# Kernel optimization log

Hardware: AMD Instinct MI355X
Metric: run time of the kernel (lower is better)

The kernel has to match this reference:

```python
import jax, jax.numpy as jnp
import numpy as np

H = 0.5
EPS = 1e-08


def setup_inputs() -> dict:
    key = jax.random.key(0)
    k1, k2, k3 = jax.random.split(key, 3)
    B, in_dim, n_rules, out_dim = 16384, 64, 128, 32
    X = jax.random.normal(k1, (B, in_dim), dtype=jnp.float32)
    centers = jax.random.normal(k2, (in_dim, n_rules), dtype=jnp.float32)
    sigmas = jnp.ones((in_dim, n_rules), dtype=jnp.float32)
    W = jax.random.normal(k3, (out_dim, (in_dim + 1) * n_rules), dtype=jnp.float32) * 0.02
    b = jnp.zeros((out_dim,), dtype=jnp.float32)
    return {"X": X, "centers": centers, "sigmas": sigmas, "W": W, "b": b}


def reference(X, centers, sigmas, W, b):
    # HTSK firing levels: mean-style scaled Gaussian log-memberships summed over in_dim
    scale = H / sigmas ** 2 + EPS                      # [in_dim, n_rules]
    diff = X[:, :, None] - centers[None, :, :]          # [B, in_dim, n_rules]
    logits = jnp.sum(-(diff ** 2) * scale, axis=1)      # [B, n_rules]
    frs = jax.nn.softmax(logits, axis=1)                # [B, n_rules]
    B = X.shape[0]
    # order=1 consequent input: rule-major outer product, then raw firing levels
    xr = (frs[:, :, None] * X[:, None, :]).reshape(B, -1)  # [B, n_rules*in_dim]
    Z = jnp.concatenate([xr, frs], axis=1)               # [B, n_rules*(in_dim+1)]
    output = Z @ W.T + b                                 # [B, out_dim]
    return output, frs
```

## Files before the change

kernel.cpp:

```cpp
#include <hip/hip_runtime.h>


#define H_CONST 0.5f
#define EPS_CONST 1e-8f
#define NROWS 16384
#define NRULES 128
#define WCOLS 8320

typedef _Float16 half8 __attribute__((ext_vector_type(8)));
typedef float floatx4 __attribute__((ext_vector_type(4)));

#define MFMA16(a, b, c) __builtin_amdgcn_mfma_f32_16x16x32_f16((a), (b), (c), 0, 0, 0)

#define WFRAG_OFF 0
#define W0FRAG_OFF 262144
#define BMAT_OFF   (262144 + 4096)
#define KVEC_BYTE_OFF 630784
#define WS_BYTES_NEEDED (630784 + 512)

__global__ __launch_bounds__(256) void prep_kernel(
    const float* __restrict__ centers, const float* __restrict__ sigmas,
    const float* __restrict__ W, _Float16* __restrict__ wsh, float* __restrict__ kvec)
{
    __shared__ float sBuf[32 * 68];
    const int t = threadIdx.x;
    const int b = blockIdx.x;

    if (b < 128) {
        const int r = b;
        {
            int o = t >> 3, seg = t & 7;
            const float* g = W + o * WCOLS + r * 64 + seg * 8;
            floatx4 a = *(const floatx4*)g;
            floatx4 c = *(const floatx4*)(g + 4);
            *(floatx4*)(sBuf + o * 68 + seg * 8) = a;
            *(floatx4*)(sBuf + o * 68 + seg * 8 + 4) = c;
        }
        __syncthreads();
        {
            int L = t & 63, nt = (t >> 6) & 1, s = t >> 7;
            int o = nt * 16 + (L & 15);
            int ib = s * 32 + ((L >> 4) & 3) * 8;
            floatx4 fa = *(const floatx4*)(sBuf + o * 68 + ib);
            floatx4 fb = *(const floatx4*)(sBuf + o * 68 + ib + 4);
            half8 h;
#pragma unroll
            for (int k = 0; k < 8; ++k) h[k] = (_Float16)((k < 4) ? fa[k & 3] : fb[k & 3]);
            *(half8*)(wsh + WFRAG_OFF + r * 2048 + t * 8) = h;
        }
    } else if (b < 136) {
        const int nt = b - 128;
        float* sS = sBuf;
        float* sC = sBuf + 1088;
        {
            int i = t >> 2, c0 = (t & 3) * 4;
            floatx4 sg4 = *(const floatx4*)(sigmas + i * NRULES + nt * 16 + c0);
            floatx4 ct4 = *(const floatx4*)(centers + i * NRULES + nt * 16 + c0);
#pragma unroll
            for (int k = 0; k < 4; ++k) { sS[i * 17 + c0 + k] = sg4[k]; sC[i * 17 + c0 + k] = ct4[k]; }
        }
        __syncthreads();
#pragma unroll
        for (int kk = 0; kk < 3; ++kk) {
            int unit = t + kk * 256;
            int s = unit >> 6, L = unit & 63;
            int q = (L >> 4) & 3, nl = L & 15;
            int g = s >> 1;
            int i0 = (s & 1) * 32 + q * 8;
            half8 h;
#pragma unroll
            for (int j = 0; j < 8; ++j) {
                int i = i0 + j;
                float sg = sS[i * 17 + nl];
                float S = H_CONST / (sg * sg) + EPS_CONST;
                float c = sC[i * 17 + nl];
                float CS2 = 2.0f * c * S;
                _Float16 v;
                if (g == 0 || g == 2) v = -(_Float16)S;
                else if (g == 1) { _Float16 sh = (_Float16)S; v = -(_Float16)(S - (float)sh); }
                else if (g == 3 || g == 5) v = (_Float16)CS2;
                else { _Float16 ch = (_Float16)CS2; v = (_Float16)(CS2 - (float)ch); }
                h[j] = v;
            }
            *(half8*)(wsh + BMAT_OFF + ((s * 8 + nt) * 64 + L) * 8) = h;
        }
    } else {
#pragma unroll
        for (int kk = 0; kk < 2; ++kk) {
            int unit = t + kk * 256;
            int s = unit >> 7, nt = (unit >> 6) & 1, L = unit & 63;
            int q = (L >> 4) & 3;
            int o = nt * 16 + (L & 15);
            half8 h;
#pragma unroll
            for (int j = 0; j < 8; ++j) {
                int r = s * 32 + q * 8 + j;
                h[j] = (_Float16)W[o * WCOLS + 8192 + r];
            }
            *(half8*)(wsh + W0FRAG_OFF + ((s * 2 + nt) * 64 + L) * 8) = h;
        }
        if (t < 128) {
            int r = t;
            float acc = 0.f;
#pragma unroll 8
            for (int i = 0; i < 64; ++i) {
                float sg = sigmas[i * NRULES + r];
                float S = H_CONST / (sg * sg) + EPS_CONST;
                float c = centers[i * NRULES + r];
                acc += c * c * S;
            }
            kvec[r] = acc;
        }
    }
}

__global__ __launch_bounds__(256) void main_fused(
    const float* __restrict__ X, const float* __restrict__ bias,
    const _Float16* __restrict__ wsh, const float* __restrict__ kvec,
    float* __restrict__ out, float* __restrict__ frs_out)
{
    __shared__ _Float16 sXh[32 * 64];
    __shared__ _Float16 sXl[32 * 64];
    __shared__ _Float16 sX2h[32 * 64];
    __shared__ _Float16 sX2l[32 * 64];
    __shared__ float sU[32 * 132];
    __shared__ _Float16 sF[32 * 136];

    const int t = threadIdx.x;
    const int w = t >> 6;
    const int L = t & 63;
    const int m = L & 15;
    const int q = L >> 4;
    const int row0 = blockIdx.x * 32;

    {
        int row = t >> 3, uc = t & 7;
        const float* gx = X + (row0 + row) * 64 + uc * 8;
        floatx4 xa = *(const floatx4*)gx;
        floatx4 xb = *(const floatx4*)(gx + 4);
        int base = row * 64 + (uc ^ (row & 7)) * 8;
        half8 vh, vl, v2h, v2l;
#pragma unroll
        for (int k = 0; k < 8; ++k) {
            float x = (k < 4) ? xa[k & 3] : xb[k & 3];
            _Float16 xh = (_Float16)x;
            _Float16 xl2 = (_Float16)(x - (float)xh);
            float x2 = x * x;
            _Float16 x2h = (_Float16)x2;
            _Float16 x2l = (_Float16)(x2 - (float)x2h);
            vh[k] = xh; vl[k] = xl2; v2h[k] = x2h; v2l[k] = x2l;
        }
        *(half8*)(sXh + base) = vh;
        *(half8*)(sXl + base) = vl;
        *(half8*)(sX2h + base) = v2h;
        *(half8*)(sX2l + base) = v2l;
    }
    __syncthreads();

    floatx4 lacc[2][2];
#pragma unroll
    for (int mt = 0; mt < 2; ++mt)
#pragma unroll
        for (int n = 0; n < 2; ++n) lacc[mt][n] = (floatx4){0.f, 0.f, 0.f, 0.f};

    const _Float16* Bm = wsh + BMAT_OFF;
#pragma unroll
    for (int s = 0; s < 12; ++s) {
        const _Float16* arr = (s < 4) ? sX2h : (s < 6) ? sX2l : (s < 10) ? sXh : sXl;
        int phys = (((s & 1) << 2) | q) ^ (m & 7);
        half8 b0 = *(const half8*)(Bm + ((s * 8 + 2 * w + 0) * 64 + L) * 8);
        half8 b1 = *(const half8*)(Bm + ((s * 8 + 2 * w + 1) * 64 + L) * 8);
#pragma unroll
        for (int mt = 0; mt < 2; ++mt) {
            half8 a = *(const half8*)(arr + (mt * 16 + m) * 64 + phys * 8);
            lacc[mt][0] = MFMA16(a, b0, lacc[mt][0]);
            lacc[mt][1] = MFMA16(a, b1, lacc[mt][1]);
        }
    }
    float kv0 = kvec[(2 * w + 0) * 16 + m];
    float kv1 = kvec[(2 * w + 1) * 16 + m];

#pragma unroll
    for (int mt = 0; mt < 2; ++mt)
#pragma unroll
        for (int ntl = 0; ntl < 2; ++ntl)
#pragma unroll
            for (int reg = 0; reg < 4; ++reg) {
                int rl = mt * 16 + q * 4 + reg;
                int col = (2 * w + ntl) * 16 + m;
                sU[rl * 132 + col] = lacc[mt][ntl][reg] - (ntl ? kv1 : kv0);
            }
    __syncthreads();

    {
        int row = t >> 3, l8 = t & 7;
        int base = row * 132 + l8 * 16;
        float v[16];
        float mx = -1e30f;
#pragma unroll
        for (int k = 0; k < 16; ++k) { v[k] = sU[base + k]; mx = fmaxf(mx, v[k]); }
        mx = fmaxf(mx, __shfl_xor(mx, 1));
        mx = fmaxf(mx, __shfl_xor(mx, 2));
        mx = fmaxf(mx, __shfl_xor(mx, 4));
        float sum = 0.f;
#pragma unroll
        for (int k = 0; k < 16; ++k) { v[k] = __expf(v[k] - mx); sum += v[k]; }
        sum += __shfl_xor(sum, 1);
        sum += __shfl_xor(sum, 2);
        sum += __shfl_xor(sum, 4);
        float inv = 1.0f / sum;
        float* gf = frs_out + (row0 + row) * 128 + l8 * 16;
        half8 h0, h1;
#pragma unroll
        for (int c = 0; c < 4; ++c) {
            floatx4 o4;
#pragma unroll
            for (int k = 0; k < 4; ++k) {
                float f = v[c * 4 + k] * inv;
                o4[k] = f;
                if (c < 2) h0[c * 4 + k] = (_Float16)f; else h1[(c - 2) * 4 + k] = (_Float16)f;
            }
            *(floatx4*)(gf + c * 4) = o4;
        }
        *(half8*)(sF + row * 136 + l8 * 16) = h0;
        *(half8*)(sF + row * 136 + l8 * 16 + 8) = h1;
    }
    __syncthreads();

    const int mt = w & 1;
    const int rh = w >> 1;

    half8 xf[2];
#pragma unroll
    for (int s = 0; s < 2; ++s) {
        int phys = ((s << 2) | q) ^ (m & 7);
        xf[s] = *(const half8*)(sXh + (mt * 16 + m) * 64 + phys * 8);
    }

    floatx4 oacc[2];
    oacc[0] = (floatx4){0.f, 0.f, 0.f, 0.f};
    oacc[1] = (floatx4){0.f, 0.f, 0.f, 0.f};

    const _Float16* Wf = wsh + WFRAG_OFF;
    const _Float16* W0f = wsh + W0FRAG_OFF;
    const int rowi = mt * 16 + m;

#pragma unroll 4
    for (int rr = 0; rr < 64; ++rr) {
        int r = rh * 64 + rr;
        const _Float16* bp = Wf + r * 2048;
        half8 b00 = *(const half8*)(bp + (0 * 64 + L) * 8);
        half8 b01 = *(const half8*)(bp + (1 * 64 + L) * 8);
        half8 b10 = *(const half8*)(bp + (2 * 64 + L) * 8);
        half8 b11 = *(const half8*)(bp + (3 * 64 + L) * 8);
        _Float16 f = sF[rowi * 136 + r];
        half8 fs;
#pragma unroll
        for (int k = 0; k < 8; ++k) fs[k] = f;
        half8 a0 = fs * xf[0];
        half8 a1 = fs * xf[1];
        oacc[0] = MFMA16(a0, b00, oacc[0]);
        oacc[0] = MFMA16(a1, b10, oacc[0]);
        oacc[1] = MFMA16(a0, b01, oacc[1]);
        oacc[1] = MFMA16(a1, b11, oacc[1]);
    }

#pragma unroll
    for (int sg = 0; sg < 2; ++sg) {
        int s = 2 * rh + sg;
        half8 a = *(const half8*)(sF + rowi * 136 + s * 32 + q * 8);
        half8 b0 = *(const half8*)(W0f + ((s * 2 + 0) * 64 + L) * 8);
        half8 b1 = *(const half8*)(W0f + ((s * 2 + 1) * 64 + L) * 8);
        oacc[0] = MFMA16(a, b0, oacc[0]);
        oacc[1] = MFMA16(a, b1, oacc[1]);
    }

    float* sR = sU;
    if (rh == 1) {
#pragma unroll
        for (int ntl = 0; ntl < 2; ++ntl)
#pragma unroll
            for (int reg = 0; reg < 4; ++reg)
                sR[(mt * 16 + q * 4 + reg) * 33 + ntl * 16 + m] = oacc[ntl][reg];
    }
    __syncthreads();
    if (rh == 0) {
        float b0 = bias[m];
        float b1 = bias[16 + m];
#pragma unroll
        for (int ntl = 0; ntl < 2; ++ntl) {
            float bb = ntl ? b1 : b0;
#pragma unroll
            for (int reg = 0; reg < 4; ++reg) {
                int rloc = mt * 16 + q * 4 + reg;
                int col = ntl * 16 + m;
                float vv = oacc[ntl][reg] + sR[rloc * 33 + col] + bb;
                out[(row0 + rloc) * 32 + col] = vv;
            }
        }
    }
}

extern "C" void kernel_launch(void* const* d_in, const int* in_sizes, int n_in,
                              void* d_out, int out_size, void* d_ws, size_t ws_size,
                              hipStream_t stream) {
    const float* X = (const float*)d_in[0];
    const float* centers = (const float*)d_in[1];
    const float* sigmas = (const float*)d_in[2];
    const float* W = (const float*)d_in[3];
    const float* b = (const float*)d_in[4];
    float* outp = (float*)d_out;
    float* frs_out = outp + NROWS * 32;
    if (ws_size < (size_t)WS_BYTES_NEEDED) return;
    _Float16* wsh = (_Float16*)d_ws;
    float* kvec = (float*)((char*)d_ws + KVEC_BYTE_OFF);

    prep_kernel<<<137, 256, 0, stream>>>(centers, sigmas, W, wsh, kvec);
    main_fused<<<NROWS / 32, 256, 0, stream>>>(X, b, wsh, kvec, outp, frs_out);
}
```

Measured before the change: 92.85 us.

## Split rules across four waves with both row tiles per wave and W prefetch

```diff
diff --git a/kernel.cpp b/kernel.cpp
--- a/kernel.cpp
+++ b/kernel.cpp
@@ -20,7 +20,7 @@
 
 __global__ __launch_bounds__(256) void prep_kernel(
     const float* __restrict__ centers, const float* __restrict__ sigmas,
-    const float* __restrict__ W, _Float16* __restrict__ wsh, float* __restrict__ kvec)
+    const float* __restrict__ W, _Float16* __restrict__ wsh)
 {
     __shared__ float sBuf[32 * 68];
     const int t = threadIdx.x;
@@ -99,19 +99,23 @@
             }
             *(half8*)(wsh + W0FRAG_OFF + ((s * 2 + nt) * 64 + L) * 8) = h;
         }
-        if (t < 128) {
-            int r = t;
-            float acc = 0.f;
+    }
+}
+
+__global__ __launch_bounds__(128) void prep_kvec(
+    const float* __restrict__ centers, const float* __restrict__ sigmas,
+    float* __restrict__ kvec)
+{
+    int r = threadIdx.x;
+    float acc = 0.f;
 #pragma unroll 8
-            for (int i = 0; i < 64; ++i) {
-                float sg = sigmas[i * NRULES + r];
-                float S = H_CONST / (sg * sg) + EPS_CONST;
-                float c = centers[i * NRULES + r];
-                acc += c * c * S;
-            }
-            kvec[r] = acc;
-        }
-    }
+    for (int i = 0; i < 64; ++i) {
+        float sg = sigmas[i * NRULES + r];
+        float S = H_CONST / (sg * sg) + EPS_CONST;
+        float c = centers[i * NRULES + r];
+        acc += c * c * S;
+    }
+    kvec[r] = acc;
 }
 
 __global__ __launch_bounds__(256) void main_fused(
@@ -123,8 +127,8 @@
     __shared__ _Float16 sXl[32 * 64];
     __shared__ _Float16 sX2h[32 * 64];
     __shared__ _Float16 sX2l[32 * 64];
-    __shared__ float sU[32 * 132];
     __shared__ _Float16 sF[32 * 136];
+    __shared__ float sU[4608];
 
     const int t = threadIdx.x;
     const int w = t >> 6;
@@ -227,78 +231,90 @@
     }
     __syncthreads();
 
-    const int mt = w & 1;
-    const int rh = w >> 1;
-
-    half8 xf[2];
-#pragma unroll
-    for (int s = 0; s < 2; ++s) {
-        int phys = ((s << 2) | q) ^ (m & 7);
-        xf[s] = *(const half8*)(sXh + (mt * 16 + m) * 64 + phys * 8);
-    }
-
-    floatx4 oacc[2];
-    oacc[0] = (floatx4){0.f, 0.f, 0.f, 0.f};
-    oacc[1] = (floatx4){0.f, 0.f, 0.f, 0.f};
-
+    const int rq = w;
+    const int r0 = rq * 32;
     const _Float16* Wf = wsh + WFRAG_OFF;
     const _Float16* W0f = wsh + W0FRAG_OFF;
-    const int rowi = mt * 16 + m;
-
-#pragma unroll 4
-    for (int rr = 0; rr < 64; ++rr) {
-        int r = rh * 64 + rr;
-        const _Float16* bp = Wf + r * 2048;
-        half8 b00 = *(const half8*)(bp + (0 * 64 + L) * 8);
-        half8 b01 = *(const half8*)(bp + (1 * 64 + L) * 8);
-        half8 b10 = *(const half8*)(bp + (2 * 64 + L) * 8);
-        half8 b11 = *(const half8*)(bp + (3 * 64 + L) * 8);
-        _Float16 f = sF[rowi * 136 + r];
-        half8 fs;
-#pragma unroll
-        for (int k = 0; k < 8; ++k) fs[k] = f;
-        half8 a0 = fs * xf[0];
-        half8 a1 = fs * xf[1];
-        oacc[0] = MFMA16(a0, b00, oacc[0]);
-        oacc[0] = MFMA16(a1, b10, oacc[0]);
-        oacc[1] = MFMA16(a0, b01, oacc[1]);
-        oacc[1] = MFMA16(a1, b11, oacc[1]);
-    }
-
-#pragma unroll
-    for (int sg = 0; sg < 2; ++sg) {
-        int s = 2 * rh + sg;
-        half8 a = *(const half8*)(sF + rowi * 136 + s * 32 + q * 8);
-        half8 b0 = *(const half8*)(W0f + ((s * 2 + 0) * 64 + L) * 8);
-        half8 b1 = *(const half8*)(W0f + ((s * 2 + 1) * 64 + L) * 8);
-        oacc[0] = MFMA16(a, b0, oacc[0]);
-        oacc[1] = MFMA16(a, b1, oacc[1]);
-    }
-
-    float* sR = sU;
-    if (rh == 1) {
+
+#define LDW(r, slot) (*(const half8*)(Wf + (r) * 2048 + ((slot) * 64 + L) * 8))
+
+    half8 xf[2][2];
+#pragma unroll
+    for (int mt = 0; mt < 2; ++mt)
+#pragma unroll
+        for (int s = 0; s < 2; ++s) {
+            int phys = ((s << 2) | q) ^ (m & 7);
+            xf[mt][s] = *(const half8*)(sXh + (mt * 16 + m) * 64 + phys * 8);
+        }
+
+    floatx4 oacc[2][2];
+#pragma unroll
+    for (int mt = 0; mt < 2; ++mt)
+#pragma unroll
+        for (int n = 0; n < 2; ++n) oacc[mt][n] = (floatx4){0.f, 0.f, 0.f, 0.f};
+
+    half8 b00 = LDW(r0, 0), b01 = LDW(r0, 1), b10 = LDW(r0, 2), b11 = LDW(r0, 3);
+
+#pragma unroll
+    for (int rg = 0; rg < 4; ++rg) {
+        half8 fv0 = *(const half8*)(sF + (0 * 16 + m) * 136 + r0 + rg * 8);
+        half8 fv1 = *(const half8*)(sF + (1 * 16 + m) * 136 + r0 + rg * 8);
+#pragma unroll
+        for (int rr2 = 0; rr2 < 8; ++rr2) {
+            half8 c00 = b00, c01 = b01, c10 = b10, c11 = b11;
+            if (rg * 8 + rr2 < 31) {
+                int rn = r0 + rg * 8 + rr2 + 1;
+                b00 = LDW(rn, 0); b01 = LDW(rn, 1); b10 = LDW(rn, 2); b11 = LDW(rn, 3);
+            }
+            _Float16 f0 = fv0[rr2], f1 = fv1[rr2];
+            half8 fs0, fs1;
+#pragma unroll
+            for (int k = 0; k < 8; ++k) { fs0[k] = f0; fs1[k] = f1; }
+            half8 a00 = fs0 * xf[0][0];
+            half8 a01 = fs0 * xf[0][1];
+            half8 a10 = fs1 * xf[1][0];
+            half8 a11 = fs1 * xf[1][1];
+            oacc[0][0] = MFMA16(a00, c00, oacc[0][0]);
+            oacc[0][0] = MFMA16(a01, c10, oacc[0][0]);
+            oacc[0][1] = MFMA16(a00, c01, oacc[0][1]);
+            oacc[0][1] = MFMA16(a01, c11, oacc[0][1]);
+            oacc[1][0] = MFMA16(a10, c00, oacc[1][0]);
+            oacc[1][0] = MFMA16(a11, c10, oacc[1][0]);
+            oacc[1][1] = MFMA16(a10, c01, oacc[1][1]);
+            oacc[1][1] = MFMA16(a11, c11, oacc[1][1]);
+        }
+    }
+
+    {
+        half8 wb0 = *(const half8*)(W0f + ((rq * 2 + 0) * 64 + L) * 8);
+        half8 wb1 = *(const half8*)(W0f + ((rq * 2 + 1) * 64 + L) * 8);
+#pragma unroll
+        for (int mt = 0; mt < 2; ++mt) {
+            half8 a = *(const half8*)(sF + (mt * 16 + m) * 136 + rq * 32 + q * 8);
+            oacc[mt][0] = MFMA16(a, wb0, oacc[mt][0]);
+            oacc[mt][1] = MFMA16(a, wb1, oacc[mt][1]);
+        }
+    }
+
+#pragma unroll
+    for (int mt = 0; mt < 2; ++mt)
 #pragma unroll
         for (int ntl = 0; ntl < 2; ++ntl)
 #pragma unroll
             for (int reg = 0; reg < 4; ++reg)
-                sR[(mt * 16 + q * 4 + reg) * 33 + ntl * 16 + m] = oacc[ntl][reg];
-    }
+                sU[w * 1152 + (mt * 16 + q * 4 + reg) * 36 + ntl * 16 + m] = oacc[mt][ntl][reg];
     __syncthreads();
-    if (rh == 0) {
-        float b0 = bias[m];
-        float b1 = bias[16 + m];
-#pragma unroll
-        for (int ntl = 0; ntl < 2; ++ntl) {
-            float bb = ntl ? b1 : b0;
-#pragma unroll
-            for (int reg = 0; reg < 4; ++reg) {
-                int rloc = mt * 16 + q * 4 + reg;
-                int col = ntl * 16 + m;
-                float vv = oacc[ntl][reg] + sR[rloc * 33 + col] + bb;
-                out[(row0 + rloc) * 32 + col] = vv;
-            }
-        }
-    }
+
+    {
+        int row = t >> 3, col0 = (t & 7) * 4;
+        floatx4 acc = *(const floatx4*)(sU + 0 * 1152 + row * 36 + col0);
+        acc += *(const floatx4*)(sU + 1 * 1152 + row * 36 + col0);
+        acc += *(const floatx4*)(sU + 2 * 1152 + row * 36 + col0);
+        acc += *(const floatx4*)(sU + 3 * 1152 + row * 36 + col0);
+        acc += *(const floatx4*)(bias + col0);
+        *(floatx4*)(out + (row0 + row) * 32 + col0) = acc;
+    }
+#undef LDW
 }
 
 extern "C" void kernel_launch(void* const* d_in, const int* in_sizes, int n_in,
@@ -315,6 +331,7 @@
     _Float16* wsh = (_Float16*)d_ws;
     float* kvec = (float*)((char*)d_ws + KVEC_BYTE_OFF);
 
-    prep_kernel<<<137, 256, 0, stream>>>(centers, sigmas, W, wsh, kvec);
+    prep_kernel<<<137, 256, 0, stream>>>(centers, sigmas, W, wsh);
+    prep_kvec<<<1, 128, 0, stream>>>(centers, sigmas, kvec);
     main_fused<<<NROWS / 32, 256, 0, stream>>>(X, b, wsh, kvec, outp, frs_out);
 }
```

Measured after the change: 91.04 us. About the same (-1.9%).
